# Performance work log

Measured on AMD Instinct MI355X. Metric: run time of the kernel, lower is better.

The kernel has to match this reference:

```python
import jax, jax.numpy as jnp
import numpy as np

B, IDIM, ODIM, MSIZE = 8192, 4096, 4096, 128
ICOUNT = (IDIM + MSIZE - 1) // MSIZE        # 32
MCOUNT = (max(IDIM, ODIM) + MSIZE - 1) // MSIZE  # 32
OCOUNT = (ODIM + MSIZE - 1) // MSIZE        # 32


def setup_inputs() -> dict:
    key = jax.random.key(0)
    ks = jax.random.split(key, 7)
    s_in = 1.0 / np.sqrt(ICOUNT)
    s_m = 1.0 / np.sqrt(MSIZE)
    s_out = 1.0 / np.sqrt(MCOUNT)
    return {
        "x": jax.random.normal(ks[0], (B, IDIM), dtype=jnp.float32),
        "W_in": jax.random.normal(ks[1], (MCOUNT, ICOUNT), dtype=jnp.float32) * s_in,
        "b_in": jax.random.normal(ks[2], (MCOUNT,), dtype=jnp.float32) * s_in,
        "W_mods": jax.random.normal(ks[3], (MCOUNT, MSIZE, MSIZE), dtype=jnp.float32) * s_m,
        "b_mods": jax.random.normal(ks[4], (MCOUNT, MSIZE), dtype=jnp.float32) * s_m,
        "W_out": jax.random.normal(ks[5], (OCOUNT, MCOUNT), dtype=jnp.float32) * s_out,
        "b_out": jax.random.normal(ks[6], (OCOUNT,), dtype=jnp.float32) * s_out,
        "odim": ODIM,
    }


def reference(x, W_in, b_in, W_mods, b_mods, W_out, b_out, odim):
    msize = W_mods.shape[-1]
    b = x.shape[0]
    idim = x.shape[-1]
    rem = idim % msize  # static
    if rem != 0:
        x = jnp.pad(x, ((0, 0), (0, msize - rem)))
    icount = x.shape[-1] // msize
    # reshape to blocks then tail_permute (swap last two axes)
    x = x.reshape(b, icount, msize).swapaxes(-1, -2)      # [B, msize, icount]
    x = jnp.einsum('bmi,ci->bmc', x, W_in) + b_in          # fcin -> [B, msize, mcount]
    x = x.swapaxes(-1, -2)                                 # [B, mcount, msize]
    # per-block submodule: Linear(msize->msize) per block, vectorized over blocks
    x = jnp.einsum('bcm,cnm->bcn', x, W_mods) + b_mods     # [B, mcount, msize]
    x = x.swapaxes(-1, -2)                                 # [B, msize, mcount]
    x = jnp.einsum('bmc,oc->bmo', x, W_out) + b_out        # fcout -> [B, msize, ocount]
    x = x.reshape(b, -1)[:, :odim]                         # [B, odim]
    return x  # act = Identity
```

## Files before the change

### kernel.cpp

```cpp
#include <hip/hip_runtime.h>
#include <hip/hip_bf16.h>
#include <stdint.h>


#define BT    16
#define NTHR  512
#define GRID  512
#define IDIM  4096
#define ODIM  4096

typedef __attribute__((ext_vector_type(8))) __bf16 bf16x8;
typedef __attribute__((ext_vector_type(4))) float  floatx4;

union BF8 { uint32_t w[4]; unsigned short h[8]; bf16x8 v; };

__device__ __forceinline__ unsigned short f2bf(float f) {
    uint32_t u = __builtin_bit_cast(uint32_t, f);
    u += 0x7fffu + ((u >> 16) & 1u);
    return (unsigned short)(u >> 16);
}

#define YP_BT 132
#define YP_C  2116
#define WP_BT 36
#define WP_N  584
#define SCR_ELEMS (16 * WP_N)

template<bool WBF16>
__global__ __launch_bounds__(NTHR, 1)
void tinymod_fused(const float* __restrict__ x,
                   const float* __restrict__ W_in,
                   const float* __restrict__ b_in,
                   const void*  __restrict__ wmods,
                   const float* __restrict__ b_mods,
                   const float* __restrict__ W_out,
                   const float* __restrict__ b_out,
                   float* __restrict__ out)
{
    __shared__ unsigned short ylds[32 * YP_C] __attribute__((aligned(16)));
    __shared__ unsigned short scr[SCR_ELEMS]  __attribute__((aligned(16)));

    const int tid  = threadIdx.x;
    const int lane = tid & 63;
    const int wave = tid >> 6;
    const int l15  = lane & 15;
    const int grp  = lane >> 4;
    const int row0 = blockIdx.x * BT;

    const float bin0 = b_in[l15],  bin1 = b_in[16 + l15];
    const float bo0  = b_out[l15], bo1  = b_out[16 + l15];
    BF8 winf[2], woutf[2];
    #pragma unroll
    for (int cc = 0; cc < 2; cc++) {
        const float* p = W_in  + (l15 + 16*cc) * 32 + grp * 8;
        const float* q = W_out + (l15 + 16*cc) * 32 + grp * 8;
        #pragma unroll
        for (int j = 0; j < 8; j++) { winf[cc].h[j] = f2bf(p[j]); woutf[cc].h[j] = f2bf(q[j]); }
    }

    const int smp = tid & 15;
    const int sbt = (tid >> 4) & 15;
    const int sih = tid >> 8;
    const float* xb = x + (row0 + sbt) * IDIM + smp;

    float xr[16];
    #pragma unroll
    for (int p = 0; p < 2; p++) {
        const int i0 = (sih + 2*p) * 8;
        #pragma unroll
        for (int j = 0; j < 8; j++) xr[p*8 + j] = xb[(i0 + j) * 128];
    }

    for (int mb = 0; mb < 8; mb++) {
        #pragma unroll
        for (int p = 0; p < 2; p++) {
            const int i0 = (sih + 2*p) * 8;
            BF8 t;
            #pragma unroll
            for (int j = 0; j < 8; j++) t.h[j] = f2bf(xr[p*8 + j]);
            uint4 val; val.x = t.w[0]; val.y = t.w[1]; val.z = t.w[2]; val.w = t.w[3];
            *(uint4*)&scr[(smp*16 + sbt)*32 + i0] = val;
        }
        __syncthreads();

        float xr2[16];
        if (mb < 7) {
            #pragma unroll
            for (int p = 0; p < 2; p++) {
                const int i0 = (sih + 2*p) * 8;
                #pragma unroll
                for (int j = 0; j < 8; j++) xr2[p*8 + j] = xb[(i0 + j) * 128 + (mb + 1) * 16];
            }
        }

        unsigned short yh[2][2][4];
        #pragma unroll
        for (int mm = 0; mm < 2; mm++) {
            const int mp = 2*wave + mm;
            BF8 a;
            const uint4 av = *(const uint4*)&scr[(mp*16 + l15)*32 + grp*8];
            a.w[0] = av.x; a.w[1] = av.y; a.w[2] = av.z; a.w[3] = av.w;
            #pragma unroll
            for (int cc = 0; cc < 2; cc++) {
                floatx4 acc = {0.f, 0.f, 0.f, 0.f};
                acc = __builtin_amdgcn_mfma_f32_16x16x32_bf16(a.v, winf[cc].v, acc, 0, 0, 0);
                const float bi = cc ? bin1 : bin0;
                #pragma unroll
                for (int r = 0; r < 4; r++) yh[mm][cc][r] = f2bf(acc[r] + bi);
            }
        }
        #pragma unroll
        for (int cc = 0; cc < 2; cc++)
            #pragma unroll
            for (int r = 0; r < 4; r++) {
                const int c  = l15 + 16*cc;
                const int bt = grp*4 + r;
                const uint32_t pk = (uint32_t)yh[0][cc][r] | ((uint32_t)yh[1][cc][r] << 16);
                *(uint32_t*)&ylds[c*YP_C + bt*YP_BT + mb*16 + 2*wave] = pk;
            }
        __syncthreads();
        if (mb < 7) {
            #pragma unroll
            for (int q = 0; q < 16; q++) xr[q] = xr2[q];
        }
    }

    const unsigned short* __restrict__ wm16 = (const unsigned short*)wmods;
    const float*          __restrict__ wm32 = (const float*)wmods;

    for (int nb = 0; nb < 8; nb++) {
        floatx4 acc[4];
        float   bm[4];
        #pragma unroll
        for (int ci = 0; ci < 4; ci++) {
            const int c = 4*wave + ci;
            bm[ci] = b_mods[c*128 + nb*16 + l15];
            const int ybase = c*YP_C + l15*YP_BT + grp*8;
            const int wbase = (c*128 + nb*16 + l15)*128 + grp*8;
            floatx4 s = {0.f, 0.f, 0.f, 0.f};
            #pragma unroll
            for (int kc = 0; kc < 4; kc++) {
                BF8 a;
                const uint2 u0 = *(const uint2*)&ylds[ybase + kc*32];
                const uint2 u1 = *(const uint2*)&ylds[ybase + kc*32 + 4];
                a.w[0] = u0.x; a.w[1] = u0.y; a.w[2] = u1.x; a.w[3] = u1.y;
                BF8 b;
                if (WBF16) {
                    const uint4 bv = *(const uint4*)&wm16[wbase + kc*32];
                    b.w[0] = bv.x; b.w[1] = bv.y; b.w[2] = bv.z; b.w[3] = bv.w;
                } else {
                    const float* wp = wm32 + wbase + kc*32;
                    #pragma unroll
                    for (int j = 0; j < 8; j++) b.h[j] = f2bf(wp[j]);
                }
                s = __builtin_amdgcn_mfma_f32_16x16x32_bf16(a.v, b.v, s, 0, 0, 0);
            }
            acc[ci] = s;
        }
        #pragma unroll
        for (int r = 0; r < 4; r++) {
            unsigned short h[4];
            #pragma unroll
            for (int ci = 0; ci < 4; ci++) h[ci] = f2bf(acc[ci][r] + bm[ci]);
            uint2 pk;
            pk.x = (uint32_t)h[0] | ((uint32_t)h[1] << 16);
            pk.y = (uint32_t)h[2] | ((uint32_t)h[3] << 16);
            *(uint2*)&scr[l15*WP_N + (grp*4 + r)*WP_BT + 4*wave] = pk;
        }
        __syncthreads();

        #pragma unroll
        for (int mm = 0; mm < 2; mm++) {
            const int mp = 2*wave + mm;
            BF8 a;
            const int off = mp*WP_N + l15*WP_BT + grp*8;
            const uint2 u0 = *(const uint2*)&scr[off];
            const uint2 u1 = *(const uint2*)&scr[off + 4];
            a.w[0] = u0.x; a.w[1] = u0.y; a.w[2] = u1.x; a.w[3] = u1.y;
            #pragma unroll
            for (int oc = 0; oc < 2; oc++) {
                floatx4 v = {0.f, 0.f, 0.f, 0.f};
                v = __builtin_amdgcn_mfma_f32_16x16x32_bf16(a.v, woutf[oc].v, v, 0, 0, 0);
                const float bo = oc ? bo1 : bo0;
                float* po = out + row0*ODIM + (nb*16 + mp)*32 + l15 + 16*oc;
                #pragma unroll
                for (int r = 0; r < 4; r++) {
                    const int bt = grp*4 + r;
                    po[bt*ODIM] = v[r] + bo;
                }
            }
        }
        __syncthreads();
    }
}

__global__ void wmods_to_bf16(const float* __restrict__ w, unsigned short* __restrict__ o) {
    const int i = (blockIdx.x * 256 + threadIdx.x) * 4;
    const float4 f = *(const float4*)(w + i);
    uint2 pk;
    pk.x = (uint32_t)f2bf(f.x) | ((uint32_t)f2bf(f.y) << 16);
    pk.y = (uint32_t)f2bf(f.z) | ((uint32_t)f2bf(f.w) << 16);
    *(uint2*)(o + i) = pk;
}

extern "C" void kernel_launch(void* const* d_in, const int* in_sizes, int n_in,
                              void* d_out, int out_size, void* d_ws, size_t ws_size,
                              hipStream_t stream)
{
    const float* x     = (const float*)d_in[0];
    const float* W_in  = (const float*)d_in[1];
    const float* b_in  = (const float*)d_in[2];
    const float* Wm    = (const float*)d_in[3];
    const float* b_m   = (const float*)d_in[4];
    const float* W_out = (const float*)d_in[5];
    const float* b_out = (const float*)d_in[6];
    float* out = (float*)d_out;

    const size_t wm_elems = 32u * 128u * 128u;
    if (ws_size >= wm_elems * sizeof(unsigned short)) {
        unsigned short* wbf = (unsigned short*)d_ws;
        wmods_to_bf16<<<(int)(wm_elems / (256 * 4)), 256, 0, stream>>>(Wm, wbf);
        tinymod_fused<true><<<GRID, NTHR, 0, stream>>>(x, W_in, b_in, (const void*)wbf,
                                                       b_m, W_out, b_out, out);
    } else {
        tinymod_fused<false><<<GRID, NTHR, 0, stream>>>(x, W_in, b_in, (const void*)Wm,
                                                        b_m, W_out, b_out, out);
    }
}
```

Measured before the change: 312.8 us.

## Restructure fused kernel to 1024 threads, accumulating module GEMM across input chunks in registers

Reorganizes the fused kernel to 16 waves per block. Instead of materialising the full fcin output for all 128 positions in LDS before the per-module GEMM, it streams 4 chunks of 32 positions: each chunk computes fcin and then immediately contributes a K-slice to register-resident accumulators for the module matmul (2 modules x 8 n-tiles per wave). The fcout stage then uses a double-buffered LDS scratch, which removes the trailing barrier per tile. This cuts LDS footprint and the number of barriers and gives more waves to hide latency, in exchange for much higher register pressure from 64 accumulator floats per lane.

```diff
diff --git a/kernel.cpp b/kernel.cpp
--- a/kernel.cpp
+++ b/kernel.cpp
@@ -1,10 +1,9 @@
 #include <hip/hip_runtime.h>
-#include <hip/hip_bf16.h>
 #include <stdint.h>
 
 
 #define BT    16
-#define NTHR  512
+#define NTHR  1024
 #define GRID  512
 #define IDIM  4096
 #define ODIM  4096
@@ -20,14 +19,16 @@
     return (unsigned short)(u >> 16);
 }
 
-#define YP_BT 132
-#define YP_C  2116
-#define WP_BT 36
-#define WP_N  584
-#define SCR_ELEMS (16 * WP_N)
+#define XP_BT 40
+#define XP_M  656
+#define YP_BT 40
+#define YP_C  648
+#define WP_BT 34
+#define WP_N  546
+#define WBUF  8736
 
 template<bool WBF16>
-__global__ __launch_bounds__(NTHR, 1)
+__global__ __launch_bounds__(NTHR, 4)
 void tinymod_fused(const float* __restrict__ x,
                    const float* __restrict__ W_in,
                    const float* __restrict__ b_in,
@@ -37,166 +38,156 @@
                    const float* __restrict__ b_out,
                    float* __restrict__ out)
 {
-    __shared__ unsigned short ylds[32 * YP_C] __attribute__((aligned(16)));
-    __shared__ unsigned short scr[SCR_ELEMS]  __attribute__((aligned(16)));
+    __shared__ unsigned short xs[32 * XP_M] __attribute__((aligned(16)));
+    __shared__ unsigned short ys[32 * YP_C] __attribute__((aligned(16)));
+    __shared__ unsigned short wc[2 * WBUF]  __attribute__((aligned(16)));
 
     const int tid  = threadIdx.x;
+    const int w    = tid >> 6;
     const int lane = tid & 63;
-    const int wave = tid >> 6;
     const int l15  = lane & 15;
     const int grp  = lane >> 4;
     const int row0 = blockIdx.x * BT;
 
-    const float bin0 = b_in[l15],  bin1 = b_in[16 + l15];
-    const float bo0  = b_out[l15], bo1  = b_out[16 + l15];
-    BF8 winf[2], woutf[2];
-    #pragma unroll
-    for (int cc = 0; cc < 2; cc++) {
-        const float* p = W_in  + (l15 + 16*cc) * 32 + grp * 8;
-        const float* q = W_out + (l15 + 16*cc) * 32 + grp * 8;
-        #pragma unroll
-        for (int j = 0; j < 8; j++) { winf[cc].h[j] = f2bf(p[j]); woutf[cc].h[j] = f2bf(q[j]); }
-    }
-
-    const int smp = tid & 15;
-    const int sbt = (tid >> 4) & 15;
-    const int sih = tid >> 8;
-    const float* xb = x + (row0 + sbt) * IDIM + smp;
-
-    float xr[16];
-    #pragma unroll
-    for (int p = 0; p < 2; p++) {
-        const int i0 = (sih + 2*p) * 8;
-        #pragma unroll
-        for (int j = 0; j < 8; j++) xr[p*8 + j] = xb[(i0 + j) * 128];
-    }
-
-    for (int mb = 0; mb < 8; mb++) {
-        #pragma unroll
-        for (int p = 0; p < 2; p++) {
-            const int i0 = (sih + 2*p) * 8;
-            BF8 t;
-            #pragma unroll
-            for (int j = 0; j < 8; j++) t.h[j] = f2bf(xr[p*8 + j]);
-            uint4 val; val.x = t.w[0]; val.y = t.w[1]; val.z = t.w[2]; val.w = t.w[3];
-            *(uint4*)&scr[(smp*16 + sbt)*32 + i0] = val;
-        }
-        __syncthreads();
-
-        float xr2[16];
-        if (mb < 7) {
-            #pragma unroll
-            for (int p = 0; p < 2; p++) {
-                const int i0 = (sih + 2*p) * 8;
-                #pragma unroll
-                for (int j = 0; j < 8; j++) xr2[p*8 + j] = xb[(i0 + j) * 128 + (mb + 1) * 16];
-            }
-        }
-
-        unsigned short yh[2][2][4];
-        #pragma unroll
-        for (int mm = 0; mm < 2; mm++) {
-            const int mp = 2*wave + mm;
-            BF8 a;
-            const uint4 av = *(const uint4*)&scr[(mp*16 + l15)*32 + grp*8];
-            a.w[0] = av.x; a.w[1] = av.y; a.w[2] = av.z; a.w[3] = av.w;
-            #pragma unroll
-            for (int cc = 0; cc < 2; cc++) {
-                floatx4 acc = {0.f, 0.f, 0.f, 0.f};
-                acc = __builtin_amdgcn_mfma_f32_16x16x32_bf16(a.v, winf[cc].v, acc, 0, 0, 0);
-                const float bi = cc ? bin1 : bin0;
-                #pragma unroll
-                for (int r = 0; r < 4; r++) yh[mm][cc][r] = f2bf(acc[r] + bi);
-            }
-        }
-        #pragma unroll
-        for (int cc = 0; cc < 2; cc++)
-            #pragma unroll
-            for (int r = 0; r < 4; r++) {
-                const int c  = l15 + 16*cc;
-                const int bt = grp*4 + r;
-                const uint32_t pk = (uint32_t)yh[0][cc][r] | ((uint32_t)yh[1][cc][r] << 16);
-                *(uint32_t*)&ylds[c*YP_C + bt*YP_BT + mb*16 + 2*wave] = pk;
-            }
-        __syncthreads();
-        if (mb < 7) {
-            #pragma unroll
-            for (int q = 0; q < 16; q++) xr[q] = xr2[q];
-        }
-    }
+    const int cc = w >> 3, mq = w & 7;
+
+    BF8 winf;
+    {
+        const float* p = W_in + (l15 + 16*cc) * 32 + grp * 8;
+        #pragma unroll
+        for (int j = 0; j < 8; j++) winf.h[j] = f2bf(p[j]);
+    }
+    const float bin = b_in[l15 + 16*cc];
+
+    const int smp = tid & 31, sbt = (tid >> 5) & 15, sih = tid >> 9;
+    const float* xb = x + (row0 + sbt) * IDIM + smp + sih * (16 * 128);
+
+    floatx4 acc[2][8];
+    #pragma unroll
+    for (int a = 0; a < 2; a++)
+        #pragma unroll
+        for (int b = 0; b < 8; b++) acc[a][b] = (floatx4){0.f, 0.f, 0.f, 0.f};
 
     const unsigned short* __restrict__ wm16 = (const unsigned short*)wmods;
     const float*          __restrict__ wm32 = (const float*)wmods;
-
-    for (int nb = 0; nb < 8; nb++) {
-        floatx4 acc[4];
-        float   bm[4];
-        #pragma unroll
-        for (int ci = 0; ci < 4; ci++) {
-            const int c = 4*wave + ci;
-            bm[ci] = b_mods[c*128 + nb*16 + l15];
-            const int ybase = c*YP_C + l15*YP_BT + grp*8;
-            const int wbase = (c*128 + nb*16 + l15)*128 + grp*8;
-            floatx4 s = {0.f, 0.f, 0.f, 0.f};
-            #pragma unroll
-            for (int kc = 0; kc < 4; kc++) {
-                BF8 a;
-                const uint2 u0 = *(const uint2*)&ylds[ybase + kc*32];
-                const uint2 u1 = *(const uint2*)&ylds[ybase + kc*32 + 4];
-                a.w[0] = u0.x; a.w[1] = u0.y; a.w[2] = u1.x; a.w[3] = u1.y;
+    int wmb[2];
+    #pragma unroll
+    for (int c2 = 0; c2 < 2; c2++)
+        wmb[c2] = ((2*w + c2) * 128 + l15) * 128 + grp * 8;
+
+    float xr[16];
+    #pragma unroll
+    for (int j = 0; j < 16; j++) xr[j] = xb[j * 128];
+
+    #pragma unroll
+    for (int mc = 0; mc < 4; mc++) {
+        #pragma unroll
+        for (int p = 0; p < 2; p++) {
+            BF8 t;
+            #pragma unroll
+            for (int j = 0; j < 8; j++) t.h[j] = f2bf(xr[p*8 + j]);
+            uint4 v4; v4.x = t.w[0]; v4.y = t.w[1]; v4.z = t.w[2]; v4.w = t.w[3];
+            *(uint4*)&xs[smp*XP_M + sbt*XP_BT + sih*16 + p*8] = v4;
+        }
+        __syncthreads();
+
+        unsigned short yh[4][4];
+        #pragma unroll
+        for (int k = 0; k < 4; k++) {
+            BF8 a;
+            const uint4 av = *(const uint4*)&xs[(mq*4 + k)*XP_M + l15*XP_BT + grp*8];
+            a.w[0] = av.x; a.w[1] = av.y; a.w[2] = av.z; a.w[3] = av.w;
+            floatx4 y = {0.f, 0.f, 0.f, 0.f};
+            y = __builtin_amdgcn_mfma_f32_16x16x32_bf16(a.v, winf.v, y, 0, 0, 0);
+            #pragma unroll
+            for (int r = 0; r < 4; r++) yh[k][r] = f2bf(y[r] + bin);
+        }
+        #pragma unroll
+        for (int r = 0; r < 4; r++) {
+            uint2 pk;
+            pk.x = (uint32_t)yh[0][r] | ((uint32_t)yh[1][r] << 16);
+            pk.y = (uint32_t)yh[2][r] | ((uint32_t)yh[3][r] << 16);
+            *(uint2*)&ys[(l15 + 16*cc)*YP_C + (grp*4 + r)*YP_BT + mq*4] = pk;
+        }
+        __syncthreads();
+
+        float xr2[16];
+        if (mc < 3) {
+            #pragma unroll
+            for (int j = 0; j < 16; j++) xr2[j] = xb[j*128 + (mc + 1)*32];
+        }
+
+        #pragma unroll
+        for (int c2 = 0; c2 < 2; c2++) {
+            BF8 a;
+            const uint4 av = *(const uint4*)&ys[(2*w + c2)*YP_C + l15*YP_BT + grp*8];
+            a.w[0] = av.x; a.w[1] = av.y; a.w[2] = av.z; a.w[3] = av.w;
+            #pragma unroll
+            for (int nt = 0; nt < 8; nt++) {
                 BF8 b;
                 if (WBF16) {
-                    const uint4 bv = *(const uint4*)&wm16[wbase + kc*32];
+                    const uint4 bv = *(const uint4*)&wm16[wmb[c2] + nt*2048 + mc*32];
                     b.w[0] = bv.x; b.w[1] = bv.y; b.w[2] = bv.z; b.w[3] = bv.w;
                 } else {
-                    const float* wp = wm32 + wbase + kc*32;
+                    const float* wp = wm32 + wmb[c2] + nt*2048 + mc*32;
                     #pragma unroll
                     for (int j = 0; j < 8; j++) b.h[j] = f2bf(wp[j]);
                 }
-                s = __builtin_amdgcn_mfma_f32_16x16x32_bf16(a.v, b.v, s, 0, 0, 0);
+                acc[c2][nt] = __builtin_amdgcn_mfma_f32_16x16x32_bf16(a.v, b.v, acc[c2][nt], 0, 0, 0);
             }
-            acc[ci] = s;
-        }
+        }
+        if (mc < 3) {
+            #pragma unroll
+            for (int j = 0; j < 16; j++) xr[j] = xr2[j];
+        }
+    }
+
+    BF8 woutf[2];
+    #pragma unroll
+    for (int oc = 0; oc < 2; oc++) {
+        const float* q = W_out + (l15 + 16*oc) * 32 + grp * 8;
+        #pragma unroll
+        for (int j = 0; j < 8; j++) woutf[oc].h[j] = f2bf(q[j]);
+    }
+    const float bo0 = b_out[l15], bo1 = b_out[16 + l15];
+    float bm[2][8];
+    #pragma unroll
+    for (int c2 = 0; c2 < 2; c2++)
+        #pragma unroll
+        for (int nt = 0; nt < 8; nt++)
+            bm[c2][nt] = b_mods[(2*w + c2)*128 + nt*16 + l15];
+
+    float* outb = out + (long)row0 * ODIM;
+    #pragma unroll
+    for (int nt = 0; nt < 8; nt++) {
+        const int buf = (nt & 1) * WBUF;
         #pragma unroll
         for (int r = 0; r < 4; r++) {
-            unsigned short h[4];
-            #pragma unroll
-            for (int ci = 0; ci < 4; ci++) h[ci] = f2bf(acc[ci][r] + bm[ci]);
-            uint2 pk;
-            pk.x = (uint32_t)h[0] | ((uint32_t)h[1] << 16);
-            pk.y = (uint32_t)h[2] | ((uint32_t)h[3] << 16);
-            *(uint2*)&scr[l15*WP_N + (grp*4 + r)*WP_BT + 4*wave] = pk;
+            const uint32_t pk = (uint32_t)f2bf(acc[0][nt][r] + bm[0][nt])
+                              | ((uint32_t)f2bf(acc[1][nt][r] + bm[1][nt]) << 16);
+            *(uint32_t*)&wc[buf + l15*WP_N + (grp*4 + r)*WP_BT + 2*w] = pk;
         }
         __syncthreads();
-
-        #pragma unroll
-        for (int mm = 0; mm < 2; mm++) {
-            const int mp = 2*wave + mm;
-            BF8 a;
-            const int off = mp*WP_N + l15*WP_BT + grp*8;
-            const uint2 u0 = *(const uint2*)&scr[off];
-            const uint2 u1 = *(const uint2*)&scr[off + 4];
-            a.w[0] = u0.x; a.w[1] = u0.y; a.w[2] = u1.x; a.w[3] = u1.y;
-            #pragma unroll
-            for (int oc = 0; oc < 2; oc++) {
-                floatx4 v = {0.f, 0.f, 0.f, 0.f};
-                v = __builtin_amdgcn_mfma_f32_16x16x32_bf16(a.v, woutf[oc].v, v, 0, 0, 0);
-                const float bo = oc ? bo1 : bo0;
-                float* po = out + row0*ODIM + (nb*16 + mp)*32 + l15 + 16*oc;
-                #pragma unroll
-                for (int r = 0; r < 4; r++) {
-                    const int bt = grp*4 + r;
-                    po[bt*ODIM] = v[r] + bo;
-                }
-            }
-        }
-        __syncthreads();
-    }
-}
-
-__global__ void wmods_to_bf16(const float* __restrict__ w, unsigned short* __restrict__ o) {
+        BF8 a;
+        #pragma unroll
+        for (int j = 0; j < 4; j++)
+            a.w[j] = *(const uint32_t*)&wc[buf + w*WP_N + l15*WP_BT + grp*8 + j*2];
+        #pragma unroll
+        for (int oc = 0; oc < 2; oc++) {
+            floatx4 v = {0.f, 0.f, 0.f, 0.f};
+            v = __builtin_amdgcn_mfma_f32_16x16x32_bf16(a.v, woutf[oc].v, v, 0, 0, 0);
+            const float bo = oc ? bo1 : bo0;
+            float* po = outb + (nt*16 + w)*32 + oc*16 + l15;
+            #pragma unroll
+            for (int r = 0; r < 4; r++)
+                po[(grp*4 + r) * ODIM] = v[r] + bo;
+        }
+    }
+}
+
+__global__ void wmods_to_bf16(const float* __restrict__ wsrc, unsigned short* __restrict__ o) {
     const int i = (blockIdx.x * 256 + threadIdx.x) * 4;
-    const float4 f = *(const float4*)(w + i);
+    const float4 f = *(const float4*)(wsrc + i);
     uint2 pk;
     pk.x = (uint32_t)f2bf(f.x) | ((uint32_t)f2bf(f.y) << 16);
     pk.y = (uint32_t)f2bf(f.z) | ((uint32_t)f2bf(f.w) << 16);
```

Result: slower. 342.5 us (+9.5%).
